# Kernel tuning notes

Measured on AMD Instinct MI355X. Metric: run time of the kernel, lower is better.

Reference implementation:

```python
import jax, jax.numpy as jnp
import numpy as np

WD, WH, WW = 2, 7, 7
N = WD * WH * WW            # 98 tokens per window
C = 192                     # dim
H = 6                       # num_heads
HD = C // H                 # head_dim = 32
NW = 512                    # number of windows per sample
B = 4                       # batch
B_ = B * NW                 # 2048 windows total
TABLE = (2 * WD - 1) * (2 * WH - 1) * (2 * WW - 1)  # 507


def _relative_position_index():
    d, h, w = np.meshgrid(np.arange(WD), np.arange(WH), np.arange(WW), indexing='ij')
    coords = np.stack([d, h, w]).reshape(3, -1)              # (3, N)
    rel = coords[:, :, None] - coords[:, None, :]            # (3, N, N)
    rel = rel.transpose(1, 2, 0).astype(np.int64)            # (N, N, 3)
    rel[:, :, 0] += WD - 1
    rel[:, :, 1] += WH - 1
    rel[:, :, 2] += WW - 1
    rel[:, :, 0] *= (2 * WH - 1) * (2 * WW - 1)
    rel[:, :, 1] *= 2 * WW - 1
    return jnp.asarray(rel.sum(-1), dtype=jnp.int32)         # (N, N)


def setup_inputs() -> dict:
    key = jax.random.key(0)
    ks = jax.random.split(key, 7)
    return {
        'x': jax.random.normal(ks[0], (B_, N, C), dtype=jnp.float32),
        'mask': jax.random.normal(ks[1], (NW, N, N), dtype=jnp.float32),
        'qkv_w': jax.random.normal(ks[2], (3 * C, C), dtype=jnp.float32) * 0.02,
        'qkv_b': jnp.zeros((3 * C,), dtype=jnp.float32),
        'proj_w': jax.random.normal(ks[3], (C, C), dtype=jnp.float32) * 0.02,
        'proj_b': jnp.zeros((C,), dtype=jnp.float32),
        'rpb_table': jax.random.normal(ks[4], (TABLE, H), dtype=jnp.float32) * 0.02,
        'rel_pos_index': _relative_position_index(),
    }


def reference(x, mask, qkv_w, qkv_b, proj_w, proj_b, rpb_table, rel_pos_index):
    Bw, n, c = x.shape
    hd = c // H
    scale = hd ** -0.5
    qkv = (x @ qkv_w.T + qkv_b).reshape(Bw, n, 3, H, hd)
    q, k, v = qkv[:, :, 0], qkv[:, :, 1], qkv[:, :, 2]       # (Bw, n, H, hd)
    # attn = (q @ k^T) * scale  (scale applied after matmul, as in source)
    attn = jnp.einsum('bihd,bjhd->bhij', q, k) * scale       # (Bw, H, n, n)
    bias = rpb_table[rel_pos_index]                          # (n, n, H)
    attn = attn + jnp.transpose(bias, (2, 0, 1))[None]       # broadcast over Bw
    nw = mask.shape[0]
    attn = attn.reshape(Bw // nw, nw, H, n, n) + mask[None, :, None]
    attn = jax.nn.softmax(attn.reshape(Bw, H, n, n), axis=-1)
    out = jnp.einsum('bhij,bjhd->bihd', attn, v).reshape(Bw, n, c)
    return out @ proj_w.T + proj_b
```

## Files before the change

### kernel.cpp

```cpp
#include <hip/hip_runtime.h>
#include <hip/hip_bf16.h>

using bf16   = __bf16;
using bf16x4 = __attribute__((ext_vector_type(4))) __bf16;
using bf16x8 = __attribute__((ext_vector_type(8))) __bf16;
using f32x4  = __attribute__((ext_vector_type(4))) float;
using f16x4  = __attribute__((ext_vector_type(4))) _Float16;

#define B_TOT 2048
#define NTOK  98
#define CDIM  192
#define NHEAD 6
#define HDIM  32
#define NWIN  512
#define NN    (NTOK*NTOK)
#define QKV_ELEMS ((size_t)B_TOT*NHEAD*NTOK*HDIM)
#define MROWS 200704
#define SCALE 0.17677669529663687f

#define MFMA(a,b,c) __builtin_amdgcn_mfma_f32_16x16x32_bf16((a),(b),(c),0,0,0)

#define GLD16(gp, lp) __builtin_amdgcn_global_load_lds(                        \
    (const __attribute__((address_space(1))) void*)(gp),                       \
    (__attribute__((address_space(3))) void*)(lp), 16, 0, 0)

__global__ void build_bias(const float* __restrict__ table,
                           const int* __restrict__ rel,
                           float* __restrict__ bias) {
    int t = blockIdx.x * 256 + threadIdx.x;
    if (t < NN) {
        int idx = rel[t];
        #pragma unroll
        for (int h = 0; h < NHEAD; ++h)
            bias[h * NN + t] = table[idx * NHEAD + h];
    }
}

__global__ void conv_swz(const float* __restrict__ src, bf16* __restrict__ dst,
                         int nchunk) {
    int t = blockIdx.x * 256 + threadIdx.x;
    if (t < nchunk) {
        int row = t / 24, c = t % 24;
        const float* s = src + (size_t)row * CDIM + c * 8;
        bf16x8 o;
        #pragma unroll
        for (int e = 0; e < 8; ++e) o[e] = (bf16)s[e];
        *(bf16x8*)(dst + (size_t)row * CDIM + ((c ^ (row & 7)) << 3)) = o;
    }
}

__global__ __launch_bounds__(256) void qkv_gemm(
    const float* __restrict__ x, const bf16* __restrict__ wb,
    const float* __restrict__ bvec,
    bf16* __restrict__ qdst, bf16* __restrict__ kdst, bf16* __restrict__ vdst)
{
    __shared__ char Bs[2][24576];
    const int tid = threadIdx.x, lane = tid & 63, wv = tid >> 6;
    const int l15 = lane & 15, l16 = lane >> 4;
    const int m0 = blockIdx.x * 64;

    {
        const char* bsrc = (const char*)wb;
        #pragma unroll
        for (int j = 0; j < 6; ++j) {
            const int ch = wv * 6 + j;
            GLD16(bsrc + ch * 1024 + lane * 16, Bs[0] + ch * 1024);
        }
    }

    const int arow = wv * 16 + l15;
    const int grow = m0 + arow;
    const float* xr = x + (size_t)grow * CDIM + l16 * 8;
    bf16x8 af[6];
    #pragma unroll
    for (int ks = 0; ks < 6; ++ks) {
        float4 v0 = *(const float4*)(xr + ks * 32);
        float4 v1 = *(const float4*)(xr + ks * 32 + 4);
        bf16x8 a;
        a[0] = (bf16)v0.x; a[1] = (bf16)v0.y; a[2] = (bf16)v0.z; a[3] = (bf16)v0.w;
        a[4] = (bf16)v1.x; a[5] = (bf16)v1.y; a[6] = (bf16)v1.z; a[7] = (bf16)v1.w;
        af[ks] = a;
    }

    __syncthreads();

    const int rowoff = (grow / NTOK) * 18816 + (grow % NTOK) * 32;
    const f32x4 z4 = {0.f, 0.f, 0.f, 0.f};

    #pragma unroll
    for (int nc = 0; nc < 9; ++nc) {
        if (nc < 8) {
            const char* bsrc = (const char*)wb + (size_t)(nc + 1) * 24576;
            #pragma unroll
            for (int j = 0; j < 6; ++j) {
                const int ch = wv * 6 + j;
                GLD16(bsrc + ch * 1024 + lane * 16, Bs[(nc + 1) & 1] + ch * 1024);
            }
        }

        f32x4 acc[4];
        #pragma unroll
        for (int ct = 0; ct < 4; ++ct) acc[ct] = z4;

        #pragma unroll
        for (int ks = 0; ks < 6; ++ks) {
            #pragma unroll
            for (int ct = 0; ct < 4; ++ct) {
                const int brow = ct * 16 + l15;
                bf16x8 bf = *(const bf16x8*)(Bs[nc & 1] + brow * 384
                                             + (((ks * 4 + l16) ^ (brow & 7)) << 4));
                acc[ct] = MFMA(bf, af[ks], acc[ct]);
            }
        }

        #pragma unroll
        for (int ct = 0; ct < 4; ++ct) {
            const int g0    = nc * 64 + ct * 16;
            const int which = g0 / CDIM;
            const int cm    = g0 % CDIM;
            const int h     = cm >> 5, hd0 = cm & 31;
            const float4 bvf = *(const float4*)(bvec + g0 + l16 * 4);
            bf16x4 s;
            #pragma unroll
            for (int r = 0; r < 4; ++r) {
                float v = acc[ct][r] + ((const float*)&bvf)[r];
                if (which == 0) v *= SCALE;
                s[r] = (bf16)v;
            }
            bf16* dp = (which == 0) ? qdst : (which == 1) ? kdst : vdst;
            *(bf16x4*)(dp + rowoff + h * 3136 + hd0 + l16 * 4) = s;
        }
        __syncthreads();
    }
}

__global__ __launch_bounds__(448) void attn_fused(
    const bf16* __restrict__ q, const bf16* __restrict__ k,
    const bf16* __restrict__ v,
    const float* __restrict__ mask, const float* __restrict__ bias,
    bf16* __restrict__ ao)
{
    __shared__ char lds[8192 + 28672 + 512];
    char* Vt = lds;
    char* P  = lds + 8192;
    float* invS = (float*)(lds + 8192 + 28672);

    const int bid = blockIdx.x;
    const int wh  = (bid & 7) * 384 + (bid >> 3);
    const int w = wh / NHEAD, h = wh % NHEAD;
    const int tid = threadIdx.x, lane = tid & 63, it = tid >> 6;
    const int l15 = lane & 15, l16 = lane >> 4;

    for (int f = tid; f < 32 * 30; f += 448) {
        int hd = f / 30, n = 98 + f % 30;
        *(bf16*)(Vt + hd * 256 + (((n >> 3) ^ (hd & 7)) << 4) + ((n & 7) << 1)) = (bf16)0.f;
    }
    {
        int zr = it * 16 + l15;
        int zc = 112 + l16 * 4;
        *(unsigned long long*)(P + zr * 256 + (((zc >> 3) ^ (zr & 7)) << 4) + ((zc & 7) << 1)) = 0ull;
    }

    const float* mrow = mask + (size_t)w * NN;
    const float* brow = bias + (size_t)h * NN;
    f16x4 mbh[7];
    #pragma unroll
    for (int r = 0; r < 4; ++r) {
        int i = it * 16 + l16 * 4 + r; if (i > 97) i = 97;
        #pragma unroll
        for (int jt = 0; jt < 7; ++jt) {
            int j = jt * 16 + l15;
            float val = (j < NTOK) ? (mrow[i * NTOK + j] + brow[i * NTOK + j])
                                   : -__builtin_inff();
            mbh[jt][r] = (_Float16)val;
        }
    }

    const int vn  = (tid >> 2) > 97 ? 97 : (tid >> 2);
    const int vh0 = (tid & 3) * 8;

    int qrow = it * 16 + l15; if (qrow > 97) qrow = 97;
    const f32x4 z4 = {0.f, 0.f, 0.f, 0.f};

    #pragma unroll 1
    for (int rep = 0; rep < 4; ++rep) {
        const int b = rep * NWIN + w;
        const size_t bho = (size_t)(b * NHEAD + h) * 3136;

        bf16x8 vv = *(const bf16x8*)(v + bho + vn * 32 + vh0);

        const bf16* qsrc = q + bho;
        const bf16* ksrc = k + bho;
        const bf16x8 qf = *(const bf16x8*)(qsrc + qrow * HDIM + l16 * 8);
        f32x4 acc[7];
        #pragma unroll
        for (int jt = 0; jt < 7; ++jt) {
            int kr = jt * 16 + l15; if (kr > 97) kr = 97;
            bf16x8 kf = *(const bf16x8*)(ksrc + kr * HDIM + l16 * 8);
            acc[jt] = MFMA(qf, kf, z4);
        }

        if (tid < 392) {
            #pragma unroll
            for (int e = 0; e < 8; ++e) {
                int hd = vh0 + e;
                *(bf16*)(Vt + hd * 256 + (((vn >> 3) ^ (hd & 7)) << 4) + ((vn & 7) << 1)) = vv[e];
            }
        }

        #pragma unroll
        for (int r = 0; r < 4; ++r) {
            float s = 0.f;
            #pragma unroll
            for (int jt = 0; jt < 7; ++jt) {
                float e = __expf(acc[jt][r] + (float)mbh[jt][r]);
                acc[jt][r] = e; s += e;
            }
            s += __shfl_xor(s, 1, 16);
            s += __shfl_xor(s, 2, 16);
            s += __shfl_xor(s, 4, 16);
            s += __shfl_xor(s, 8, 16);
            if (l15 == 0) invS[it * 16 + l16 * 4 + r] = 1.f / s;
        }

        #pragma unroll
        for (int jt = 0; jt < 7; ++jt) {
            #pragma unroll
            for (int r = 0; r < 4; ++r) {
                int row = it * 16 + l16 * 4 + r;
                int j = jt * 16 + l15;
                *(bf16*)(P + row * 256 + (((j >> 3) ^ (row & 7)) << 4) + ((j & 7) << 1))
                    = (bf16)acc[jt][r];
            }
        }
        __syncthreads();

        f32x4 o0 = z4, o1 = z4;
        const int prow = it * 16 + l15;
        #pragma unroll
        for (int ks = 0; ks < 4; ++ks) {
            int kchunk = ks * 4 + l16;
            bf16x8 pf = *(const bf16x8*)(P + prow * 256 + ((kchunk ^ (prow & 7)) << 4));
            bf16x8 v0 = *(const bf16x8*)(Vt + l15 * 256 + ((kchunk ^ (l15 & 7)) << 4));
            bf16x8 v1 = *(const bf16x8*)(Vt + (16 + l15) * 256 + ((kchunk ^ (l15 & 7)) << 4));
            o0 = MFMA(v0, pf, o0);
            o1 = MFMA(v1, pf, o1);
        }

        {
            int row = it * 16 + l15;
            if (row < NTOK) {
                float inv = invS[row];
                bf16* dst = ao + (size_t)b * NTOK * CDIM;
                bf16x4 s0, s1;
                #pragma unroll
                for (int r = 0; r < 4; ++r) {
                    s0[r] = (bf16)(o0[r] * inv);
                    s1[r] = (bf16)(o1[r] * inv);
                }
                const int swr = (b * NTOK + row) & 7;
                const int c0 = h * 4 + (l16 >> 1);
                const int c1 = c0 + 2;
                const int wi = (l16 & 1) << 2;
                *(bf16x4*)(dst + (size_t)row * CDIM + (((c0 ^ swr) << 3) | wi)) = s0;
                *(bf16x4*)(dst + (size_t)row * CDIM + (((c1 ^ swr) << 3) | wi)) = s1;
            }
        }
        if (rep < 3) __syncthreads();
    }
}

__global__ __launch_bounds__(256) void proj_gemm(
    const bf16* __restrict__ ao, const bf16* __restrict__ wb,
    const float* __restrict__ bvec, float* __restrict__ out)
{
    __shared__ char As[24576];
    __shared__ char Bs[2][24576];
    const int tid = threadIdx.x, lane = tid & 63, wv = tid >> 6;
    const int l15 = lane & 15, l16 = lane >> 4;
    const int m0 = blockIdx.x * 64;

    {
        const char* asrc = (const char*)ao + (size_t)m0 * 384;
        const char* bsrc = (const char*)wb;
        #pragma unroll
        for (int j = 0; j < 6; ++j) {
            const int ch = wv * 6 + j;
            GLD16(asrc + ch * 1024 + lane * 16, As + ch * 1024);
            GLD16(bsrc + ch * 1024 + lane * 16, Bs[0] + ch * 1024);
        }
    }
    __syncthreads();

    const int arow = wv * 16 + l15;
    bf16x8 af[6];
    #pragma unroll
    for (int ks = 0; ks < 6; ++ks)
        af[ks] = *(const bf16x8*)(As + arow * 384 + (((ks * 4 + l16) ^ (arow & 7)) << 4));

    const size_t orow = (size_t)(m0 + arow) * CDIM;
    const f32x4 z4 = {0.f, 0.f, 0.f, 0.f};

    #pragma unroll
    for (int nc = 0; nc < 3; ++nc) {
        if (nc < 2) {
            const char* bsrc = (const char*)wb + (size_t)(nc + 1) * 24576;
            #pragma unroll
            for (int j = 0; j < 6; ++j) {
                const int ch = wv * 6 + j;
                GLD16(bsrc + ch * 1024 + lane * 16, Bs[(nc + 1) & 1] + ch * 1024);
            }
        }

        f32x4 acc[4];
        #pragma unroll
        for (int ct = 0; ct < 4; ++ct) acc[ct] = z4;

        #pragma unroll
        for (int ks = 0; ks < 6; ++ks) {
            #pragma unroll
            for (int ct = 0; ct < 4; ++ct) {
                const int brow = ct * 16 + l15;
                bf16x8 bf = *(const bf16x8*)(Bs[nc & 1] + brow * 384
                                             + (((ks * 4 + l16) ^ (brow & 7)) << 4));
                acc[ct] = MFMA(bf, af[ks], acc[ct]);
            }
        }

        #pragma unroll
        for (int ct = 0; ct < 4; ++ct) {
            const int g0 = nc * 64 + ct * 16;
            const float4 bvf = *(const float4*)(bvec + g0 + l16 * 4);
            f32x4 s;
            #pragma unroll
            for (int r = 0; r < 4; ++r)
                s[r] = acc[ct][r] + ((const float*)&bvf)[r];
            *(f32x4*)(out + orow + g0 + l16 * 4) = s;
        }
        __syncthreads();
    }
}

extern "C" void kernel_launch(void* const* d_in, const int* in_sizes, int n_in,
                              void* d_out, int out_size, void* d_ws, size_t ws_size,
                              hipStream_t stream)
{
    (void)in_sizes; (void)n_in; (void)out_size; (void)ws_size;
    const float* x      = (const float*)d_in[0];
    const float* mask   = (const float*)d_in[1];
    const float* qkv_w  = (const float*)d_in[2];
    const float* qkv_b  = (const float*)d_in[3];
    const float* proj_w = (const float*)d_in[4];
    const float* proj_b = (const float*)d_in[5];
    const float* rpb    = (const float*)d_in[6];
    const int*   rel    = (const int*)d_in[7];
    float* out = (float*)d_out;

    char* ws = (char*)d_ws;
    bf16* qb = (bf16*)ws;
    bf16* kb = qb + QKV_ELEMS;
    bf16* vb = kb + QKV_ELEMS;
    size_t off = 3 * QKV_ELEMS * sizeof(bf16);
    float* bias = (float*)(ws + off);
    off += ((size_t)NHEAD * NN * 4 + 255) / 256 * 256;
    bf16* ao = (bf16*)(ws + off);
    bf16* qwb = ao;
    bf16* pwb = qb;

    build_bias<<<(NN + 255) / 256, 256, 0, stream>>>(rpb, rel, bias);
    conv_swz<<<(576 * 24 + 255) / 256, 256, 0, stream>>>(qkv_w, qwb, 576 * 24);
    qkv_gemm<<<MROWS / 64, 256, 0, stream>>>(x, qwb, qkv_b, qb, kb, vb);
    attn_fused<<<NWIN * NHEAD, 448, 0, stream>>>(qb, kb, vb, mask, bias, ao);
    conv_swz<<<(192 * 24 + 255) / 256, 256, 0, stream>>>(proj_w, pwb, 192 * 24);
    proj_gemm<<<MROWS / 64, 256, 0, stream>>>(ao, pwb, proj_b, out);
}
```

Before: 335.1 us.

## Assign one wave per window-head in attention, dropping block barriers and mask reuse

The attention kernel now gives each 64-lane wave a whole (window, head) pair and loops over 7 query tiles, with per-wave private LDS for V transpose and P. Previously 7 waves shared a head across 4 batch reps, with block-wide syncs. This removes __syncthreads and keeps K in registers across query tiles. The trade-off is that mask+bias is reloaded from global per (b,h) instead of cached in f16 registers and reused across the 4 reps, which raises global and L2 traffic. It also adds serial work per wave because of the 7-iteration loop.

```diff
diff --git a/kernel.cpp b/kernel.cpp
--- a/kernel.cpp
+++ b/kernel.cpp
@@ -5,7 +5,6 @@
 using bf16x4 = __attribute__((ext_vector_type(4))) __bf16;
 using bf16x8 = __attribute__((ext_vector_type(8))) __bf16;
 using f32x4  = __attribute__((ext_vector_type(4))) float;
-using f16x4  = __attribute__((ext_vector_type(4))) _Float16;
 
 #define B_TOT 2048
 #define NTOK  98
@@ -134,113 +133,115 @@
     }
 }
 
-__global__ __launch_bounds__(448) void attn_fused(
+__global__ __launch_bounds__(256) void attn_fused(
     const bf16* __restrict__ q, const bf16* __restrict__ k,
     const bf16* __restrict__ v,
     const float* __restrict__ mask, const float* __restrict__ bias,
     bf16* __restrict__ ao)
 {
-    __shared__ char lds[8192 + 28672 + 512];
-    char* Vt = lds;
-    char* P  = lds + 8192;
-    float* invS = (float*)(lds + 8192 + 28672);
-
-    const int bid = blockIdx.x;
-    const int wh  = (bid & 7) * 384 + (bid >> 3);
-    const int w = wh / NHEAD, h = wh % NHEAD;
-    const int tid = threadIdx.x, lane = tid & 63, it = tid >> 6;
+    __shared__ char lds[4 * 8192 + 4 * 4096 + 4 * 64];
+    const int tid = threadIdx.x, lane = tid & 63, wv = tid >> 6;
     const int l15 = lane & 15, l16 = lane >> 4;
-
-    for (int f = tid; f < 32 * 30; f += 448) {
-        int hd = f / 30, n = 98 + f % 30;
+    char*  Vt   = lds + wv * 8192;
+    char*  P    = lds + 32768 + wv * 4096;
+    float* invS = (float*)(lds + 49152 + wv * 64);
+
+    const int u = blockIdx.x * 4 + wv;
+    const int b = u / NHEAD, h = u - b * NHEAD;
+    const int w = b & (NWIN - 1);
+    const size_t bho = (size_t)u * 3136;
+
+    bf16x8 vvv[7];
+    #pragma unroll
+    for (int t = 0; t < 7; ++t) {
+        int idx = t * 64 + lane;
+        int n = idx >> 2; if (n > 97) n = 97;
+        int hd0 = (idx & 3) * 8;
+        vvv[t] = *(const bf16x8*)(v + bho + n * 32 + hd0);
+    }
+
+    bf16x8 kf[7];
+    #pragma unroll
+    for (int jt = 0; jt < 7; ++jt) {
+        int kr = jt * 16 + l15; if (kr > 97) kr = 97;
+        kf[jt] = *(const bf16x8*)(k + bho + kr * HDIM + l16 * 8);
+    }
+
+    #pragma unroll
+    for (int t = 0; t < 7; ++t) {
+        int idx = t * 64 + lane;
+        if (idx < 392) {
+            int n = idx >> 2, hd0 = (idx & 3) * 8;
+            #pragma unroll
+            for (int e = 0; e < 8; ++e) {
+                int hd = hd0 + e;
+                *(bf16*)(Vt + hd * 256 + (((n >> 3) ^ (hd & 7)) << 4) + ((n & 7) << 1))
+                    = vvv[t][e];
+            }
+        }
+    }
+    #pragma unroll
+    for (int t = 0; t < 15; ++t) {
+        int idx = t * 64 + lane;
+        int hd = idx / 30, n = 98 + idx % 30;
         *(bf16*)(Vt + hd * 256 + (((n >> 3) ^ (hd & 7)) << 4) + ((n & 7) << 1)) = (bf16)0.f;
     }
     {
-        int zr = it * 16 + l15;
-        int zc = 112 + l16 * 4;
-        *(unsigned long long*)(P + zr * 256 + (((zc >> 3) ^ (zr & 7)) << 4) + ((zc & 7) << 1)) = 0ull;
+        int zr = lane >> 2;
+        int zc = 112 + (lane & 3) * 4;
+        *(unsigned long long*)(P + zr * 256 + (((zc >> 3) ^ (zr & 7)) << 4)
+                               + ((zc & 7) << 1)) = 0ull;
     }
 
     const float* mrow = mask + (size_t)w * NN;
     const float* brow = bias + (size_t)h * NN;
-    f16x4 mbh[7];
-    #pragma unroll
-    for (int r = 0; r < 4; ++r) {
-        int i = it * 16 + l16 * 4 + r; if (i > 97) i = 97;
-        #pragma unroll
-        for (int jt = 0; jt < 7; ++jt) {
-            int j = jt * 16 + l15;
-            float val = (j < NTOK) ? (mrow[i * NTOK + j] + brow[i * NTOK + j])
-                                   : -__builtin_inff();
-            mbh[jt][r] = (_Float16)val;
-        }
-    }
-
-    const int vn  = (tid >> 2) > 97 ? 97 : (tid >> 2);
-    const int vh0 = (tid & 3) * 8;
-
-    int qrow = it * 16 + l15; if (qrow > 97) qrow = 97;
+    bf16* dst = ao + (size_t)b * NTOK * CDIM;
     const f32x4 z4 = {0.f, 0.f, 0.f, 0.f};
 
     #pragma unroll 1
-    for (int rep = 0; rep < 4; ++rep) {
-        const int b = rep * NWIN + w;
-        const size_t bho = (size_t)(b * NHEAD + h) * 3136;
-
-        bf16x8 vv = *(const bf16x8*)(v + bho + vn * 32 + vh0);
-
-        const bf16* qsrc = q + bho;
-        const bf16* ksrc = k + bho;
-        const bf16x8 qf = *(const bf16x8*)(qsrc + qrow * HDIM + l16 * 8);
+    for (int it = 0; it < 7; ++it) {
+        int qrow = it * 16 + l15; if (qrow > 97) qrow = 97;
+        const bf16x8 qf = *(const bf16x8*)(q + bho + qrow * HDIM + l16 * 8);
         f32x4 acc[7];
         #pragma unroll
-        for (int jt = 0; jt < 7; ++jt) {
-            int kr = jt * 16 + l15; if (kr > 97) kr = 97;
-            bf16x8 kf = *(const bf16x8*)(ksrc + kr * HDIM + l16 * 8);
-            acc[jt] = MFMA(qf, kf, z4);
-        }
-
-        if (tid < 392) {
-            #pragma unroll
-            for (int e = 0; e < 8; ++e) {
-                int hd = vh0 + e;
-                *(bf16*)(Vt + hd * 256 + (((vn >> 3) ^ (hd & 7)) << 4) + ((vn & 7) << 1)) = vv[e];
-            }
-        }
+        for (int jt = 0; jt < 7; ++jt)
+            acc[jt] = MFMA(qf, kf[jt], z4);
 
         #pragma unroll
         for (int r = 0; r < 4; ++r) {
+            int i = it * 16 + l16 * 4 + r; if (i > 97) i = 97;
             float s = 0.f;
             #pragma unroll
             for (int jt = 0; jt < 7; ++jt) {
-                float e = __expf(acc[jt][r] + (float)mbh[jt][r]);
+                int j = jt * 16 + l15;
+                float mbv = (j < NTOK) ? (mrow[i * NTOK + j] + brow[i * NTOK + j])
+                                       : -__builtin_inff();
+                float e = __expf(acc[jt][r] + mbv);
                 acc[jt][r] = e; s += e;
             }
             s += __shfl_xor(s, 1, 16);
             s += __shfl_xor(s, 2, 16);
             s += __shfl_xor(s, 4, 16);
             s += __shfl_xor(s, 8, 16);
-            if (l15 == 0) invS[it * 16 + l16 * 4 + r] = 1.f / s;
+            if (l15 == 0) invS[l16 * 4 + r] = 1.f / s;
         }
 
         #pragma unroll
         for (int jt = 0; jt < 7; ++jt) {
             #pragma unroll
             for (int r = 0; r < 4; ++r) {
-                int row = it * 16 + l16 * 4 + r;
+                int row = l16 * 4 + r;
                 int j = jt * 16 + l15;
                 *(bf16*)(P + row * 256 + (((j >> 3) ^ (row & 7)) << 4) + ((j & 7) << 1))
                     = (bf16)acc[jt][r];
             }
         }
-        __syncthreads();
 
         f32x4 o0 = z4, o1 = z4;
-        const int prow = it * 16 + l15;
         #pragma unroll
         for (int ks = 0; ks < 4; ++ks) {
             int kchunk = ks * 4 + l16;
-            bf16x8 pf = *(const bf16x8*)(P + prow * 256 + ((kchunk ^ (prow & 7)) << 4));
+            bf16x8 pf = *(const bf16x8*)(P + l15 * 256 + ((kchunk ^ (l15 & 7)) << 4));
             bf16x8 v0 = *(const bf16x8*)(Vt + l15 * 256 + ((kchunk ^ (l15 & 7)) << 4));
             bf16x8 v1 = *(const bf16x8*)(Vt + (16 + l15) * 256 + ((kchunk ^ (l15 & 7)) << 4));
             o0 = MFMA(v0, pf, o0);
@@ -250,8 +251,7 @@
         {
             int row = it * 16 + l15;
             if (row < NTOK) {
-                float inv = invS[row];
-                bf16* dst = ao + (size_t)b * NTOK * CDIM;
+                float inv = invS[l15];
                 bf16x4 s0, s1;
                 #pragma unroll
                 for (int r = 0; r < 4; ++r) {
@@ -266,7 +266,6 @@
                 *(bf16x4*)(dst + (size_t)row * CDIM + (((c1 ^ swr) << 3) | wi)) = s1;
             }
         }
-        if (rep < 3) __syncthreads();
     }
 }
 
@@ -370,7 +369,7 @@
     build_bias<<<(NN + 255) / 256, 256, 0, stream>>>(rpb, rel, bias);
     conv_swz<<<(576 * 24 + 255) / 256, 256, 0, stream>>>(qkv_w, qwb, 576 * 24);
     qkv_gemm<<<MROWS / 64, 256, 0, stream>>>(x, qwb, qkv_b, qb, kb, vb);
-    attn_fused<<<NWIN * NHEAD, 448, 0, stream>>>(qb, kb, vb, mask, bias, ao);
+    attn_fused<<<(B_TOT * NHEAD) / 4, 256, 0, stream>>>(qb, kb, vb, mask, bias, ao);
     conv_swz<<<(192 * 24 + 255) / 256, 256, 0, stream>>>(proj_w, pwb, 192 * 24);
     proj_gemm<<<MROWS / 64, 256, 0, stream>>>(ao, pwb, proj_b, out);
 }
```

New measurement: 335.2 us. No clear change (+0.0%).
